# Optimization experiments

Hardware: AMD Instinct MI355X
Metric: run time of the kernel (lower is better)

## Reference

```python
import jax, jax.numpy as jnp
import numpy as np

# Problem-size constants (match input_specs / init_kwargs)
B, D, H, W = 2, 128, 128, 128   # batch and spatial grid
N = 200_000                      # number of active (non-empty) voxels
CI, CO, K = 64, 64, 3            # channels and cubic kernel size
DIL = 1                          # dilation


def setup_inputs() -> dict:
    key = jax.random.key(0)
    k1, k2, k3 = jax.random.split(key, 3)
    # Unique active voxel coordinates (submanifold conv assumes unique sites).
    rng = np.random.default_rng(0)
    lin = rng.choice(B * D * H * W, size=N, replace=False)
    b, rem = np.divmod(lin, D * H * W)
    z, rem = np.divmod(rem, H * W)
    y, x = np.divmod(rem, W)
    coords = jnp.asarray(np.stack([b, z, y, x], axis=1).astype(np.int32))  # [N,4]
    feats = jax.random.normal(k1, (N, CI), dtype=jnp.float32)
    # kaiming-uniform-ish init, layout [Co, Kd, Kh, Kw, Ci] as in the module
    fan_in = CI * K * K * K
    bound = 1.0 / np.sqrt(fan_in)
    weight = jax.random.uniform(k2, (CO, K, K, K, CI), dtype=jnp.float32,
                                minval=-bound, maxval=bound)
    bias = jax.random.uniform(k3, (CO,), dtype=jnp.float32,
                              minval=-bound, maxval=bound)
    return {"feats": feats, "weight": weight, "bias": bias, "coords": coords}


def _build_grid(coords):
    """Dense voxel hash: linear cell id -> row index in feats (-1 if empty)."""
    n = coords.shape[0]
    lin = ((coords[:, 0] * D + coords[:, 1]) * H + coords[:, 2]) * W + coords[:, 3]
    grid = jnp.full((B * D * H * W,), -1, dtype=jnp.int32)
    return grid.at[lin].set(jnp.arange(n, dtype=jnp.int32))


def reference(feats, weight, bias, coords):
    # Submanifold sparse 3D conv: out[p] = bias + sum_k W[k] @ feats[p + dil*(k - center)]
    # (only where the neighbor voxel is active; output sites == input sites).
    n = feats.shape[0]
    grid = _build_grid(coords)
    c = K // 2
    bz, z0, y0, x0 = coords[:, 0], coords[:, 1], coords[:, 2], coords[:, 3]
    out = jnp.broadcast_to(bias.astype(feats.dtype), (n, CO))
    for kd in range(K):
        for kh in range(K):
            for kw in range(K):
                dz, dy, dx = DIL * (kd - c), DIL * (kh - c), DIL * (kw - c)
                nz, ny, nx = z0 + dz, y0 + dy, x0 + dx
                inb = (nz >= 0) & (nz < D) & (ny >= 0) & (ny < H) & (nx >= 0) & (nx < W)
                nlin = ((bz * D + jnp.clip(nz, 0, D - 1)) * H
                        + jnp.clip(ny, 0, H - 1)) * W + jnp.clip(nx, 0, W - 1)
                nidx = jnp.where(inb, grid[nlin], -1)          # rulebook for this offset
                valid = (nidx >= 0)[:, None]
                g = jnp.where(valid, feats[jnp.clip(nidx, 0)], 0.0)  # gather [N,Ci]
                out = out + jnp.einsum('nc,oc->no', g, weight[:, kd, kh, kw, :])
    return out
```

## Files before the change

### kernel.cpp

```cpp
#include <hip/hip_runtime.h>
#include <hip/hip_bf16.h>

#define BDIM 2
#define DDIM 128
#define HDIM 128
#define WDIM 128
#define CI 64
#define CO 64
#define NTAPS 27
#define GRID_CELLS (BDIM * DDIM * HDIM * WDIM)
#define NCBLK (GRID_CELLS / 256)

typedef __attribute__((ext_vector_type(8))) short short8;
typedef __attribute__((ext_vector_type(4))) float floatx4;

#define WT_OFF   ((size_t)16 << 20)
#define BCNT_OFF (WT_OFF + ((size_t)256 << 10))
#define ORD_OFF  (BCNT_OFF + ((size_t)64 << 10))
#define ZROW_OFF (ORD_OFF + ((size_t)1 << 20))

typedef const __attribute__((address_space(1))) void* gas_t;
typedef __attribute__((address_space(3))) void* las_t;

__device__ __forceinline__ unsigned short f2bf(float f) {
    unsigned int u = __float_as_uint(f);
    return (unsigned short)((u + 0x7FFFu + ((u >> 16) & 1u)) >> 16);
}

__global__ __launch_bounds__(256) void setup_kernel(
    const int* __restrict__ coords, int* __restrict__ grid, int n,
    const float* __restrict__ weight, short8* __restrict__ wt8,
    float* __restrict__ zrow) {
    int bid = blockIdx.x, tid = threadIdx.x;
    if (bid < 54) {
        int idx = bid * 256 + tid;
        int l = idx & 63, ot = (idx >> 6) & 3, s = (idx >> 8) & 1, t = idx >> 9;
        int o = ot * 16 + (l & 15);
        int k0 = s * 32 + ((l >> 4) << 3);
        const float* src = weight + ((size_t)o * NTAPS + t) * CI + k0;
        short8 v;
#pragma unroll
        for (int j = 0; j < 8; ++j) v[j] = (short)f2bf(src[j]);
        wt8[idx] = v;
    } else if (bid == 54) {
        if (tid < 64) zrow[tid] = 0.f;
    } else {
        int i = (bid - 55) * 256 + tid;
        if (i < n) {
            int4 c = ((const int4*)coords)[i];
            grid[((c.x * DDIM + c.y) * HDIM + c.z) * WDIM + c.w] = i;
        }
    }
}

__global__ __launch_bounds__(256) void count_kernel(
    const int* __restrict__ grid, int* __restrict__ bcnt) {
    int i = blockIdx.x * 256 + threadIdx.x;
    unsigned long long b = __ballot(grid[i] >= 0);
    __shared__ int wc[4];
    if ((threadIdx.x & 63) == 0) wc[threadIdx.x >> 6] = __popcll(b);
    __syncthreads();
    if (threadIdx.x == 0) bcnt[blockIdx.x] = wc[0] + wc[1] + wc[2] + wc[3];
}

__global__ __launch_bounds__(1024) void scan_kernel(int* __restrict__ bcnt) {
    __shared__ int part[1024];
    int tid = threadIdx.x;
    int v[16], s = 0;
#pragma unroll
    for (int k = 0; k < 16; ++k) { v[k] = bcnt[tid * 16 + k]; s += v[k]; }
    part[tid] = s;
    __syncthreads();
    for (int off = 1; off < 1024; off <<= 1) {
        int t = (tid >= off) ? part[tid - off] : 0;
        __syncthreads();
        part[tid] += t;
        __syncthreads();
    }
    int ex = tid ? part[tid - 1] : 0;
#pragma unroll
    for (int k = 0; k < 16; ++k) { int nv = ex; ex += v[k]; bcnt[tid * 16 + k] = nv; }
}

__global__ __launch_bounds__(256) void emit_kernel(
    const int* __restrict__ grid, const int* __restrict__ boff,
    int* __restrict__ order) {
    int i = blockIdx.x * 256 + threadIdx.x;
    int v = grid[i];
    int lane = threadIdx.x & 63, w = threadIdx.x >> 6;
    unsigned long long b = __ballot(v >= 0);
    __shared__ int wc[4];
    if (lane == 0) wc[w] = __popcll(b);
    __syncthreads();
    int woff = 0;
    for (int k = 0; k < w; ++k) woff += wc[k];
    if (v >= 0) {
        int rank = __popcll(b & ((1ull << lane) - 1ull));
        order[boff[blockIdx.x] + woff + rank] = v;
    }
}

__global__ __launch_bounds__(256) void conv_kernel(
    const float* __restrict__ feats, const short8* __restrict__ wt8,
    const float* __restrict__ bias, const int* __restrict__ coords,
    const int* __restrict__ grid, const int* __restrict__ order,
    const float* __restrict__ zrow, float* __restrict__ out, int n) {
    __shared__ short8 bs[3][512];
    int tid = threadIdx.x;
    int w = tid >> 6, l = tid & 63, quad = l >> 4, m = l & 15;

    float b0 = bias[m], b1 = bias[m + 16], b2 = bias[m + 32], b3 = bias[m + 48];

    int jrow = blockIdx.x * 64 + w * 16 + m;
    int j = jrow < n ? jrow : n - 1;
    int p = order[j];
    int4 c = ((const int4*)coords)[p];

    int pr[7];
#pragma unroll
    for (int i = 0; i < 7; ++i) {
        int t = 4 * i + quad;
        int v = -1;
        if (t < NTAPS) {
            int dz = t / 9 - 1, rem = t % 9;
            int dy = rem / 3 - 1, dx = rem % 3 - 1;
            int nz = c.y + dz, ny = c.z + dy, nx = c.w + dx;
            if (nz >= 0 && nz < DDIM && ny >= 0 && ny < HDIM &&
                nx >= 0 && nx < WDIM)
                v = grid[((c.x * DDIM + nz) * HDIM + ny) * WDIM + nx];
        }
        pr[i] = v;
    }

    floatx4 acc0 = {0.f, 0.f, 0.f, 0.f}, acc1 = acc0, acc2 = acc0, acc3 = acc0;
    float4 x[3][4];
    int vval[3];

#define VMW(N) asm volatile("s_waitcnt vmcnt(" #N ")" ::: "memory")

#define STAGE(t)                                                              \
    {                                                                         \
        const short8* gsrc = wt8 + (size_t)(t) * 512 + w * 128 + l;           \
        __builtin_amdgcn_global_load_lds((gas_t)gsrc,                         \
            (las_t)&bs[(t) % 3][w * 128], 16, 0, 0);                          \
        __builtin_amdgcn_global_load_lds((gas_t)(gsrc + 64),                  \
            (las_t)&bs[(t) % 3][w * 128 + 64], 16, 0, 0);                     \
    }

#define GATHER(t)                                                             \
    {                                                                         \
        int vv = __shfl(pr[(t) >> 2], (((t) & 3) << 4) | m);                  \
        vval[(t) % 3] = vv;                                                   \
        const float4* ar =                                                    \
            (const float4*)(vv >= 0 ? feats + (size_t)vv * CI : zrow) +       \
            quad * 2;                                                         \
        float4* xb = x[(t) % 3];                                              \
        xb[0] = ar[0]; xb[1] = ar[1]; xb[2] = ar[8]; xb[3] = ar[9];           \
    }

#define COMPUTE(t)                                                                 \
    if (__ballot(vval[(t) % 3] >= 0) != 0ull) {                                    \
        const float4* g = x[(t) % 3];                                              \
        union { short8 s; __hip_bfloat162 h[4]; } f0, f1;                          \
        f0.h[0] = __float22bfloat162_rn({g[0].x, g[0].y});                         \
        f0.h[1] = __float22bfloat162_rn({g[0].z, g[0].w});                         \
        f0.h[2] = __float22bfloat162_rn({g[1].x, g[1].y});                         \
        f0.h[3] = __float22bfloat162_rn({g[1].z, g[1].w});                         \
        f1.h[0] = __float22bfloat162_rn({g[2].x, g[2].y});                         \
        f1.h[1] = __float22bfloat162_rn({g[2].z, g[2].w});                         \
        f1.h[2] = __float22bfloat162_rn({g[3].x, g[3].y});                         \
        f1.h[3] = __float22bfloat162_rn({g[3].z, g[3].w});                         \
        const short8* wb = &bs[(t) % 3][l];                                        \
        __builtin_amdgcn_s_setprio(1);                                             \
        acc0 = __builtin_amdgcn_mfma_f32_16x16x32_bf16(f0.s, wb[0 * 64], acc0, 0, 0, 0); \
        acc1 = __builtin_amdgcn_mfma_f32_16x16x32_bf16(f0.s, wb[1 * 64], acc1, 0, 0, 0); \
        acc2 = __builtin_amdgcn_mfma_f32_16x16x32_bf16(f0.s, wb[2 * 64], acc2, 0, 0, 0); \
        acc3 = __builtin_amdgcn_mfma_f32_16x16x32_bf16(f0.s, wb[3 * 64], acc3, 0, 0, 0); \
        acc0 = __builtin_amdgcn_mfma_f32_16x16x32_bf16(f1.s, wb[4 * 64], acc0, 0, 0, 0); \
        acc1 = __builtin_amdgcn_mfma_f32_16x16x32_bf16(f1.s, wb[5 * 64], acc1, 0, 0, 0); \
        acc2 = __builtin_amdgcn_mfma_f32_16x16x32_bf16(f1.s, wb[6 * 64], acc2, 0, 0, 0); \
        acc3 = __builtin_amdgcn_mfma_f32_16x16x32_bf16(f1.s, wb[7 * 64], acc3, 0, 0, 0); \
        __builtin_amdgcn_s_setprio(0);                                             \
    }

    STAGE(0); GATHER(0);
    STAGE(1); GATHER(1);

#pragma unroll
    for (int t = 0; t < NTAPS; ++t) {
        if (t + 2 < NTAPS) { STAGE(t + 2); GATHER(t + 2); }
        if (t < NTAPS - 2)       { VMW(12); }
        else if (t == NTAPS - 2) { VMW(6); }
        else                     { VMW(0); }
        __builtin_amdgcn_sched_barrier(0);
        __builtin_amdgcn_s_barrier();
        __builtin_amdgcn_sched_barrier(0);
        COMPUTE(t);
        __builtin_amdgcn_sched_barrier(0);
        __builtin_amdgcn_s_barrier();
    }

#pragma unroll
    for (int r = 0; r < 4; ++r) {
        int row = quad * 4 + r;
        int jr = blockIdx.x * 64 + w * 16 + row;
        int prow = __shfl(p, row);
        if (jr < n) {
            float* orow = out + (size_t)prow * CO;
            orow[m]      = acc0[r] + b0;
            orow[m + 16] = acc1[r] + b1;
            orow[m + 32] = acc2[r] + b2;
            orow[m + 48] = acc3[r] + b3;
        }
    }
#undef STAGE
#undef GATHER
#undef COMPUTE
#undef VMW
}

extern "C" void kernel_launch(void* const* d_in, const int* in_sizes, int n_in,
                              void* d_out, int out_size, void* d_ws, size_t ws_size,
                              hipStream_t stream) {
    const float* feats  = (const float*)d_in[0];
    const float* weight = (const float*)d_in[1];
    const float* bias   = (const float*)d_in[2];
    const int*   coords = (const int*)d_in[3];
    float* out = (float*)d_out;
    int n = in_sizes[3] / 4;

    int*    grid  = (int*)d_ws;
    short8* wt8   = (short8*)((char*)d_ws + WT_OFF);
    int*    bcnt  = (int*)((char*)d_ws + BCNT_OFF);
    int*    order = (int*)((char*)d_ws + ORD_OFF);
    float*  zrow  = (float*)((char*)d_ws + ZROW_OFF);

    (void)hipMemsetAsync(grid, 0xFF, (size_t)GRID_CELLS * sizeof(int), stream);
    setup_kernel<<<55 + (n + 255) / 256, 256, 0, stream>>>(
        coords, grid, n, weight, wt8, zrow);
    count_kernel<<<NCBLK, 256, 0, stream>>>(grid, bcnt);
    scan_kernel<<<1, 1024, 0, stream>>>(bcnt);
    emit_kernel<<<NCBLK, 256, 0, stream>>>(grid, bcnt, order);
    conv_kernel<<<(n + 63) / 64, 256, 0, stream>>>(
        feats, wt8, bias, coords, grid, order, zrow, out, n);
}
```

Before: 205.9 us.

## Pre-convert features to bf16, replace scan with atomic ordering, quad-buffer weights

Features are converted to bf16 once in the setup kernel, so each of the 27 neighbour gathers in the conv kernel loads half as many bytes and skips the per-tap conversion. The count and scan kernels are replaced by one atomic counter in the emit kernel, which removes two launches but makes the order of sites nondeterministic at block granularity. The weight LDS ring grows to four stages so the trailing barrier in each tap can be dropped. The bf16 path depends on the workspace being large enough and falls back to the fp32 path otherwise.

```diff
diff --git a/kernel.cpp b/kernel.cpp
--- a/kernel.cpp
+++ b/kernel.cpp
@@ -15,9 +15,10 @@
 typedef __attribute__((ext_vector_type(4))) float floatx4;
 
 #define WT_OFF   ((size_t)16 << 20)
-#define BCNT_OFF (WT_OFF + ((size_t)256 << 10))
-#define ORD_OFF  (BCNT_OFF + ((size_t)64 << 10))
+#define CNT_OFF  (WT_OFF + ((size_t)256 << 10))
+#define ORD_OFF  (CNT_OFF + ((size_t)64 << 10))
 #define ZROW_OFF (ORD_OFF + ((size_t)1 << 20))
+#define FB_OFF   ((size_t)18 << 20)
 
 typedef const __attribute__((address_space(1))) void* gas_t;
 typedef __attribute__((address_space(3))) void* las_t;
@@ -30,7 +31,8 @@
 __global__ __launch_bounds__(256) void setup_kernel(
     const int* __restrict__ coords, int* __restrict__ grid, int n,
     const float* __restrict__ weight, short8* __restrict__ wt8,
-    float* __restrict__ zrow) {
+    float* __restrict__ zrow, const float* __restrict__ feats,
+    short8* __restrict__ fb8, int nbf, int* __restrict__ counter) {
     int bid = blockIdx.x, tid = threadIdx.x;
     if (bid < 54) {
         int idx = bid * 256 + tid;
@@ -44,8 +46,18 @@
         wt8[idx] = v;
     } else if (bid == 54) {
         if (tid < 64) zrow[tid] = 0.f;
+        if (tid == 64) *counter = 0;
+    } else if (bid < 55 + nbf) {
+        int g = (bid - 55) * 256 + tid;
+        if (g < n * 8) {
+            const float* s = feats + (size_t)g * 8;
+            short8 v;
+#pragma unroll
+            for (int j = 0; j < 8; ++j) v[j] = (short)f2bf(s[j]);
+            fb8[g] = v;
+        }
     } else {
-        int i = (bid - 55) * 256 + tid;
+        int i = (bid - 55 - nbf) * 256 + tid;
         if (i < n) {
             int4 c = ((const int4*)coords)[i];
             grid[((c.x * DDIM + c.y) * HDIM + c.z) * WDIM + c.w] = i;
@@ -53,59 +65,35 @@
     }
 }
 
-__global__ __launch_bounds__(256) void count_kernel(
-    const int* __restrict__ grid, int* __restrict__ bcnt) {
-    int i = blockIdx.x * 256 + threadIdx.x;
-    unsigned long long b = __ballot(grid[i] >= 0);
-    __shared__ int wc[4];
-    if ((threadIdx.x & 63) == 0) wc[threadIdx.x >> 6] = __popcll(b);
-    __syncthreads();
-    if (threadIdx.x == 0) bcnt[blockIdx.x] = wc[0] + wc[1] + wc[2] + wc[3];
-}
-
-__global__ __launch_bounds__(1024) void scan_kernel(int* __restrict__ bcnt) {
-    __shared__ int part[1024];
-    int tid = threadIdx.x;
-    int v[16], s = 0;
-#pragma unroll
-    for (int k = 0; k < 16; ++k) { v[k] = bcnt[tid * 16 + k]; s += v[k]; }
-    part[tid] = s;
-    __syncthreads();
-    for (int off = 1; off < 1024; off <<= 1) {
-        int t = (tid >= off) ? part[tid - off] : 0;
-        __syncthreads();
-        part[tid] += t;
-        __syncthreads();
-    }
-    int ex = tid ? part[tid - 1] : 0;
-#pragma unroll
-    for (int k = 0; k < 16; ++k) { int nv = ex; ex += v[k]; bcnt[tid * 16 + k] = nv; }
-}
-
 __global__ __launch_bounds__(256) void emit_kernel(
-    const int* __restrict__ grid, const int* __restrict__ boff,
+    const int* __restrict__ grid, int* __restrict__ counter,
     int* __restrict__ order) {
     int i = blockIdx.x * 256 + threadIdx.x;
     int v = grid[i];
     int lane = threadIdx.x & 63, w = threadIdx.x >> 6;
     unsigned long long b = __ballot(v >= 0);
     __shared__ int wc[4];
+    __shared__ int base;
     if (lane == 0) wc[w] = __popcll(b);
+    __syncthreads();
+    if (threadIdx.x == 0) base = atomicAdd(counter, wc[0] + wc[1] + wc[2] + wc[3]);
     __syncthreads();
     int woff = 0;
     for (int k = 0; k < w; ++k) woff += wc[k];
     if (v >= 0) {
         int rank = __popcll(b & ((1ull << lane) - 1ull));
-        order[boff[blockIdx.x] + woff + rank] = v;
-    }
-}
-
+        order[base + woff + rank] = v;
+    }
+}
+
+template <bool BF>
 __global__ __launch_bounds__(256) void conv_kernel(
-    const float* __restrict__ feats, const short8* __restrict__ wt8,
-    const float* __restrict__ bias, const int* __restrict__ coords,
-    const int* __restrict__ grid, const int* __restrict__ order,
-    const float* __restrict__ zrow, float* __restrict__ out, int n) {
-    __shared__ short8 bs[3][512];
+    const float* __restrict__ feats, const short8* __restrict__ fb8,
+    const short8* __restrict__ wt8, const float* __restrict__ bias,
+    const int* __restrict__ coords, const int* __restrict__ grid,
+    const int* __restrict__ order, const float* __restrict__ zrow,
+    float* __restrict__ out, int n) {
+    __shared__ short8 bs[4][512];
     int tid = threadIdx.x;
     int w = tid >> 6, l = tid & 63, quad = l >> 4, m = l & 15;
 
@@ -133,7 +121,8 @@
     }
 
     floatx4 acc0 = {0.f, 0.f, 0.f, 0.f}, acc1 = acc0, acc2 = acc0, acc3 = acc0;
-    float4 x[3][4];
+    short8 xb[3][2];
+    float4 xf[3][4];
     int vval[3];
 
 #define VMW(N) asm volatile("s_waitcnt vmcnt(" #N ")" ::: "memory")
@@ -142,44 +131,58 @@
     {                                                                         \
         const short8* gsrc = wt8 + (size_t)(t) * 512 + w * 128 + l;           \
         __builtin_amdgcn_global_load_lds((gas_t)gsrc,                         \
-            (las_t)&bs[(t) % 3][w * 128], 16, 0, 0);                          \
+            (las_t)&bs[(t) & 3][w * 128], 16, 0, 0);                          \
         __builtin_amdgcn_global_load_lds((gas_t)(gsrc + 64),                  \
-            (las_t)&bs[(t) % 3][w * 128 + 64], 16, 0, 0);                     \
+            (las_t)&bs[(t) & 3][w * 128 + 64], 16, 0, 0);                     \
     }
 
 #define GATHER(t)                                                             \
     {                                                                         \
         int vv = __shfl(pr[(t) >> 2], (((t) & 3) << 4) | m);                  \
         vval[(t) % 3] = vv;                                                   \
-        const float4* ar =                                                    \
-            (const float4*)(vv >= 0 ? feats + (size_t)vv * CI : zrow) +       \
-            quad * 2;                                                         \
-        float4* xb = x[(t) % 3];                                              \
-        xb[0] = ar[0]; xb[1] = ar[1]; xb[2] = ar[8]; xb[3] = ar[9];           \
+        if constexpr (BF) {                                                   \
+            const short8* ar =                                                \
+                (vv >= 0 ? fb8 + (size_t)vv * 8 : (const short8*)zrow) + quad;\
+            xb[(t) % 3][0] = ar[0];                                           \
+            xb[(t) % 3][1] = ar[4];                                           \
+        } else {                                                              \
+            const float4* ar =                                                \
+                (const float4*)(vv >= 0 ? feats + (size_t)vv * CI : zrow) +   \
+                quad * 2;                                                     \
+            float4* xp = xf[(t) % 3];                                         \
+            xp[0] = ar[0]; xp[1] = ar[1]; xp[2] = ar[8]; xp[3] = ar[9];       \
+        }                                                                     \
     }
 
 #define COMPUTE(t)                                                                 \
     if (__ballot(vval[(t) % 3] >= 0) != 0ull) {                                    \
-        const float4* g = x[(t) % 3];                                              \
-        union { short8 s; __hip_bfloat162 h[4]; } f0, f1;                          \
-        f0.h[0] = __float22bfloat162_rn({g[0].x, g[0].y});                         \
-        f0.h[1] = __float22bfloat162_rn({g[0].z, g[0].w});                         \
-        f0.h[2] = __float22bfloat162_rn({g[1].x, g[1].y});                         \
-        f0.h[3] = __float22bfloat162_rn({g[1].z, g[1].w});                         \
-        f1.h[0] = __float22bfloat162_rn({g[2].x, g[2].y});                         \
-        f1.h[1] = __float22bfloat162_rn({g[2].z, g[2].w});                         \
-        f1.h[2] = __float22bfloat162_rn({g[3].x, g[3].y});                         \
-        f1.h[3] = __float22bfloat162_rn({g[3].z, g[3].w});                         \
-        const short8* wb = &bs[(t) % 3][l];                                        \
+        short8 f0s, f1s;                                                           \
+        if constexpr (BF) {                                                        \
+            f0s = xb[(t) % 3][0];                                                  \
+            f1s = xb[(t) % 3][1];                                                  \
+        } else {                                                                   \
+            const float4* g = xf[(t) % 3];                                         \
+            union { short8 s; __hip_bfloat162 h[4]; } f0, f1;                      \
+            f0.h[0] = __float22bfloat162_rn({g[0].x, g[0].y});                     \
+            f0.h[1] = __float22bfloat162_rn({g[0].z, g[0].w});                     \
+            f0.h[2] = __float22bfloat162_rn({g[1].x, g[1].y});                     \
+            f0.h[3] = __float22bfloat162_rn({g[1].z, g[1].w});                     \
+            f1.h[0] = __float22bfloat162_rn({g[2].x, g[2].y});                     \
+            f1.h[1] = __float22bfloat162_rn({g[2].z, g[2].w});                     \
+            f1.h[2] = __float22bfloat162_rn({g[3].x, g[3].y});                     \
+            f1.h[3] = __float22bfloat162_rn({g[3].z, g[3].w});                     \
+            f0s = f0.s; f1s = f1.s;                                                \
+        }                                                                          \
+        const short8* wb = &bs[(t) & 3][l];                                        \
         __builtin_amdgcn_s_setprio(1);                                             \
-        acc0 = __builtin_amdgcn_mfma_f32_16x16x32_bf16(f0.s, wb[0 * 64], acc0, 0, 0, 0); \
-        acc1 = __builtin_amdgcn_mfma_f32_16x16x32_bf16(f0.s, wb[1 * 64], acc1, 0, 0, 0); \
-        acc2 = __builtin_amdgcn_mfma_f32_16x16x32_bf16(f0.s, wb[2 * 64], acc2, 0, 0, 0); \
-        acc3 = __builtin_amdgcn_mfma_f32_16x16x32_bf16(f0.s, wb[3 * 64], acc3, 0, 0, 0); \
-        acc0 = __builtin_amdgcn_mfma_f32_16x16x32_bf16(f1.s, wb[4 * 64], acc0, 0, 0, 0); \
-        acc1 = __builtin_amdgcn_mfma_f32_16x16x32_bf16(f1.s, wb[5 * 64], acc1, 0, 0, 0); \
-        acc2 = __builtin_amdgcn_mfma_f32_16x16x32_bf16(f1.s, wb[6 * 64], acc2, 0, 0, 0); \
-        acc3 = __builtin_amdgcn_mfma_f32_16x16x32_bf16(f1.s, wb[7 * 64], acc3, 0, 0, 0); \
+        acc0 = __builtin_amdgcn_mfma_f32_16x16x32_bf16(f0s, wb[0 * 64], acc0, 0, 0, 0); \
+        acc1 = __builtin_amdgcn_mfma_f32_16x16x32_bf16(f0s, wb[1 * 64], acc1, 0, 0, 0); \
+        acc2 = __builtin_amdgcn_mfma_f32_16x16x32_bf16(f0s, wb[2 * 64], acc2, 0, 0, 0); \
+        acc3 = __builtin_amdgcn_mfma_f32_16x16x32_bf16(f0s, wb[3 * 64], acc3, 0, 0, 0); \
+        acc0 = __builtin_amdgcn_mfma_f32_16x16x32_bf16(f1s, wb[4 * 64], acc0, 0, 0, 0); \
+        acc1 = __builtin_amdgcn_mfma_f32_16x16x32_bf16(f1s, wb[5 * 64], acc1, 0, 0, 0); \
+        acc2 = __builtin_amdgcn_mfma_f32_16x16x32_bf16(f1s, wb[6 * 64], acc2, 0, 0, 0); \
+        acc3 = __builtin_amdgcn_mfma_f32_16x16x32_bf16(f1s, wb[7 * 64], acc3, 0, 0, 0); \
         __builtin_amdgcn_s_setprio(0);                                             \
     }
 
@@ -189,15 +192,20 @@
 #pragma unroll
     for (int t = 0; t < NTAPS; ++t) {
         if (t + 2 < NTAPS) { STAGE(t + 2); GATHER(t + 2); }
-        if (t < NTAPS - 2)       { VMW(12); }
-        else if (t == NTAPS - 2) { VMW(6); }
-        else                     { VMW(0); }
+        if constexpr (BF) {
+            if (t < NTAPS - 2)       { VMW(8); }
+            else if (t == NTAPS - 2) { VMW(4); }
+            else                     { VMW(0); }
+        } else {
+            if (t < NTAPS - 2)       { VMW(12); }
+            else if (t == NTAPS - 2) { VMW(6); }
+            else                     { VMW(0); }
+        }
         __builtin_amdgcn_sched_barrier(0);
         __builtin_amdgcn_s_barrier();
         __builtin_amdgcn_sched_barrier(0);
         COMPUTE(t);
         __builtin_amdgcn_sched_barrier(0);
-        __builtin_amdgcn_s_barrier();
     }
 
 #pragma unroll
@@ -229,18 +237,24 @@
     float* out = (float*)d_out;
     int n = in_sizes[3] / 4;
 
-    int*    grid  = (int*)d_ws;
-    short8* wt8   = (short8*)((char*)d_ws + WT_OFF);
-    int*    bcnt  = (int*)((char*)d_ws + BCNT_OFF);
-    int*    order = (int*)((char*)d_ws + ORD_OFF);
-    float*  zrow  = (float*)((char*)d_ws + ZROW_OFF);
+    int*    grid    = (int*)d_ws;
+    short8* wt8     = (short8*)((char*)d_ws + WT_OFF);
+    int*    counter = (int*)((char*)d_ws + CNT_OFF);
+    int*    order   = (int*)((char*)d_ws + ORD_OFF);
+    float*  zrow    = (float*)((char*)d_ws + ZROW_OFF);
+    short8* fb8     = (short8*)((char*)d_ws + FB_OFF);
+
+    int useBF = ws_size >= FB_OFF + (size_t)n * CI * 2;
+    int nbf = useBF ? (n * 8 + 255) / 256 : 0;
 
     (void)hipMemsetAsync(grid, 0xFF, (size_t)GRID_CELLS * sizeof(int), stream);
-    setup_kernel<<<55 + (n + 255) / 256, 256, 0, stream>>>(
-        coords, grid, n, weight, wt8, zrow);
-    count_kernel<<<NCBLK, 256, 0, stream>>>(grid, bcnt);
-    scan_kernel<<<1, 1024, 0, stream>>>(bcnt);
-    emit_kernel<<<NCBLK, 256, 0, stream>>>(grid, bcnt, order);
-    conv_kernel<<<(n + 63) / 64, 256, 0, stream>>>(
-        feats, wt8, bias, coords, grid, order, zrow, out, n);
-}
+    setup_kernel<<<55 + nbf + (n + 255) / 256, 256, 0, stream>>>(
+        coords, grid, n, weight, wt8, zrow, feats, fb8, nbf, counter);
+    emit_kernel<<<NCBLK, 256, 0, stream>>>(grid, counter, order);
+    if (useBF)
+        conv_kernel<true><<<(n + 63) / 64, 256, 0, stream>>>(
+            feats, fb8, wt8, bias, coords, grid, order, zrow, out, n);
+    else
+        conv_kernel<false><<<(n + 63) / 64, 256, 0, stream>>>(
+            feats, fb8, wt8, bias, coords, grid, order, zrow, out, n);
+}
```

Result: slower. 364.1 us (+76.9%).
